# Optimization experiments

Hardware: AMD Instinct MI355X
Metric: run time of the kernel (lower is better)

Reference implementation:

```python
import jax, jax.numpy as jnp
import numpy as np

D_MODEL = 512
NUM_HEADS = 8
DEPTH = D_MODEL // NUM_HEADS


def setup_inputs() -> dict:
    key = jax.random.key(0)
    ks = jax.random.split(key, 11)
    B, S = 2, 4096
    scale = 1.0 / np.sqrt(D_MODEL)
    inp = {
        "q": jax.random.normal(ks[0], (B, S, D_MODEL), jnp.float32),
        "k": jax.random.normal(ks[1], (B, S, D_MODEL), jnp.float32),
        "v": jax.random.normal(ks[2], (B, S, D_MODEL), jnp.float32),
        "wq_w": jax.random.normal(ks[3], (D_MODEL, D_MODEL), jnp.float32) * scale,
        "wq_b": jnp.zeros((D_MODEL,), jnp.float32),
        "wk_w": jax.random.normal(ks[4], (D_MODEL, D_MODEL), jnp.float32) * scale,
        "wk_b": jnp.zeros((D_MODEL,), jnp.float32),
        "wv_w": jax.random.normal(ks[5], (D_MODEL, D_MODEL), jnp.float32) * scale,
        "wv_b": jnp.zeros((D_MODEL,), jnp.float32),
        "wo_w": jax.random.normal(ks[6], (D_MODEL, D_MODEL), jnp.float32) * scale,
        "wo_b": jnp.zeros((D_MODEL,), jnp.float32),
    }
    return inp


def _split_heads(x):
    # [B, S, D] -> [B, H, S, depth]
    B, S, _ = x.shape
    return x.reshape(B, S, NUM_HEADS, DEPTH).transpose(0, 2, 1, 3)


def reference(q, k, v, wq_w, wq_b, wk_w, wk_b, wv_w, wv_b, wo_w, wo_b):
    B, S, _ = q.shape
    qh = _split_heads(q @ wq_w.T + wq_b)  # [B,H,S,d]
    kh = _split_heads(k @ wk_w.T + wk_b)
    vh = _split_heads(v @ wv_w.T + wv_b)
    logits = jnp.einsum('bhqd,bhkd->bhqk', qh, kh) / jnp.sqrt(
        jnp.asarray(DEPTH, jnp.float32))
    attn = jax.nn.softmax(logits, axis=-1)
    out = jnp.einsum('bhqk,bhkd->bhqd', attn, vh)  # [B,H,S,d]
    out = out.transpose(0, 2, 1, 3).reshape(B, S, D_MODEL)
    return out @ wo_w.T + wo_b
```

## Files before the change

### kernel.cpp

```cpp
#include <hip/hip_runtime.h>

typedef __attribute__((ext_vector_type(8))) short short8;
typedef __attribute__((ext_vector_type(4))) float float4v;

#define D_MODEL 512
#define NUM_HEADS 8
#define DEPTH 64
#define SEQ 4096
#define BATCH 2
#define MROWS (BATCH * SEQ)
#define SCALE_Q 0.18033688011112043f

#define SW(r, c) (((r) * 64) + ((((c) ^ ((r) & 7))) * 8))

static __device__ __forceinline__ unsigned short f2bf(float f) {
  unsigned int u = __builtin_bit_cast(unsigned int, f);
  u += 0x7FFFu + ((u >> 16) & 1u);
  return (unsigned short)(u >> 16);
}
static __device__ __forceinline__ unsigned int pk2(float a, float b) {
  return (unsigned int)f2bf(a) | ((unsigned int)f2bf(b) << 16);
}

struct CvtArgs {
  const float4v* src[7];
  uint2* dst[7];
  int n4[7];
};
__global__ __launch_bounds__(256) void cvt_all(CvtArgs a) {
  const int ti = blockIdx.y;
  const float4v* __restrict__ s = a.src[ti];
  uint2* __restrict__ d = a.dst[ti];
  const int n = a.n4[ti];
  for (int i = blockIdx.x * 256 + threadIdx.x; i < n; i += gridDim.x * 256) {
    float4v f = s[i];
    d[i] = make_uint2(pk2(f[0], f[1]), pk2(f[2], f[3]));
  }
}

struct QkvArgs {
  const void* X[3];
  const void* W[3];
  const float* bias[3];
  unsigned short* out[3];
};
template <int XFP32, int WFP32>
__global__ __launch_bounds__(256) void gemm_qkv(QkvArgs a) {
  __shared__ unsigned short As[64 * 72];
  __shared__ unsigned short Bs[64 * 72];
  const int z = blockIdx.z;
  const void* __restrict__ Xv = a.X[z];
  const void* __restrict__ Wv = a.W[z];
  const float* __restrict__ bias = a.bias[z];
  unsigned short* __restrict__ outv = a.out[z];
  const int t = threadIdx.x;
  const int w = t >> 6, l = t & 63, lq = l >> 4, lm = l & 15;
  const int mBase = blockIdx.x * 64;
  const int nBase = blockIdx.y * 64;
  float4v acc[4] = {};
  for (int kc = 0; kc < D_MODEL; kc += 64) {
    __syncthreads();
#pragma unroll
    for (int p = 0; p < 2; ++p) {
      int idx = p * 256 + t;
      int r = idx >> 3, c = (idx & 7) * 8;
      if (XFP32) {
        const float* Xf = (const float*)Xv;
        float4v f0 = *reinterpret_cast<const float4v*>(&Xf[(size_t)(mBase + r) * D_MODEL + kc + c]);
        float4v f1 = *reinterpret_cast<const float4v*>(&Xf[(size_t)(mBase + r) * D_MODEL + kc + c + 4]);
        short8 s;
#pragma unroll
        for (int j = 0; j < 4; ++j) {
          s[j] = (short)f2bf(f0[j]);
          s[4 + j] = (short)f2bf(f1[j]);
        }
        *reinterpret_cast<short8*>(&As[r * 72 + c]) = s;
      } else {
        const unsigned short* Xb = (const unsigned short*)Xv;
        *reinterpret_cast<short8*>(&As[r * 72 + c]) =
            *reinterpret_cast<const short8*>(&Xb[(size_t)(mBase + r) * D_MODEL + kc + c]);
      }
      if (WFP32) {
        const float* Wf = (const float*)Wv;
        float4v f0 = *reinterpret_cast<const float4v*>(&Wf[(size_t)(nBase + r) * D_MODEL + kc + c]);
        float4v f1 = *reinterpret_cast<const float4v*>(&Wf[(size_t)(nBase + r) * D_MODEL + kc + c + 4]);
        short8 s;
#pragma unroll
        for (int j = 0; j < 4; ++j) {
          s[j] = (short)f2bf(f0[j]);
          s[4 + j] = (short)f2bf(f1[j]);
        }
        *reinterpret_cast<short8*>(&Bs[r * 72 + c]) = s;
      } else {
        const unsigned short* Wb = (const unsigned short*)Wv;
        *reinterpret_cast<short8*>(&Bs[r * 72 + c]) =
            *reinterpret_cast<const short8*>(&Wb[(size_t)(nBase + r) * D_MODEL + kc + c]);
      }
    }
    __syncthreads();
#pragma unroll
    for (int kk = 0; kk < 64; kk += 32) {
      short8 av = *reinterpret_cast<const short8*>(&As[(w * 16 + lm) * 72 + kk + lq * 8]);
#pragma unroll
      for (int f = 0; f < 4; ++f) {
        short8 b = *reinterpret_cast<const short8*>(&Bs[(f * 16 + lm) * 72 + kk + lq * 8]);
        acc[f] = __builtin_amdgcn_mfma_f32_16x16x32_bf16(av, b, acc[f], 0, 0, 0);
      }
    }
  }
  if (z == 2) {
    __syncthreads();
    unsigned short* T = As;
#pragma unroll
    for (int f = 0; f < 4; ++f) {
      int dl = f * 16 + lm;
      float bv = bias[nBase + dl];
      uint2 u;
      u.x = pk2(acc[f][0] + bv, acc[f][1] + bv);
      u.y = pk2(acc[f][2] + bv, acc[f][3] + bv);
      int chunk = 2 * w + (lq >> 1);
      *reinterpret_cast<uint2*>(&T[SW(dl, chunk) + (lq & 1) * 4]) = u;
    }
    __syncthreads();
    const int bb = mBase >> 12, s0v = mBase & 4095, h = nBase >> 6;
    const size_t vbase = ((size_t)(bb * NUM_HEADS + h)) * DEPTH * SEQ;
#pragma unroll
    for (int p = 0; p < 2; ++p) {
      int idx = p * 256 + t;
      int d = idx >> 3, c = idx & 7;
      *reinterpret_cast<short8*>(&outv[vbase + (size_t)d * SEQ + s0v + c * 8]) =
          *reinterpret_cast<const short8*>(&T[SW(d, c)]);
    }
  } else {
    const float scale = (z == 0) ? SCALE_Q : 1.0f;
#pragma unroll
    for (int f = 0; f < 4; ++f) {
      int gn = nBase + f * 16 + lm;
      float bv = bias[gn];
#pragma unroll
      for (int r = 0; r < 4; ++r) {
        int gm = mBase + w * 16 + lq * 4 + r;
        float v = (acc[f][r] + bv) * scale;
        int bb = gm >> 12, s = gm & 4095;
        int h = gn >> 6, d = gn & 63;
        outv[(((size_t)(bb * NUM_HEADS + h) * SEQ + s) << 6) + d] = f2bf(v);
      }
    }
  }
}

template <int WFP32>
__global__ __launch_bounds__(256) void gemm_out(
    const unsigned short* __restrict__ Xb,
    const void* __restrict__ Wv,
    const float* __restrict__ bias,
    float* __restrict__ out) {
  __shared__ unsigned short As[64 * 72];
  __shared__ unsigned short Bs[64 * 72];
  const int t = threadIdx.x;
  const int w = t >> 6, l = t & 63, lq = l >> 4, lm = l & 15;
  const int mBase = blockIdx.x * 64;
  const int nBase = blockIdx.y * 64;
  float4v acc[4] = {};
  for (int kc = 0; kc < D_MODEL; kc += 64) {
    __syncthreads();
#pragma unroll
    for (int p = 0; p < 2; ++p) {
      int idx = p * 256 + t;
      int r = idx >> 3, c = (idx & 7) * 8;
      *reinterpret_cast<short8*>(&As[r * 72 + c]) =
          *reinterpret_cast<const short8*>(&Xb[(size_t)(mBase + r) * D_MODEL + kc + c]);
      if (WFP32) {
        const float* Wf = (const float*)Wv;
        float4v f0 = *reinterpret_cast<const float4v*>(&Wf[(size_t)(nBase + r) * D_MODEL + kc + c]);
        float4v f1 = *reinterpret_cast<const float4v*>(&Wf[(size_t)(nBase + r) * D_MODEL + kc + c + 4]);
        short8 s;
#pragma unroll
        for (int j = 0; j < 4; ++j) {
          s[j] = (short)f2bf(f0[j]);
          s[4 + j] = (short)f2bf(f1[j]);
        }
        *reinterpret_cast<short8*>(&Bs[r * 72 + c]) = s;
      } else {
        const unsigned short* Wb = (const unsigned short*)Wv;
        *reinterpret_cast<short8*>(&Bs[r * 72 + c]) =
            *reinterpret_cast<const short8*>(&Wb[(size_t)(nBase + r) * D_MODEL + kc + c]);
      }
    }
    __syncthreads();
#pragma unroll
    for (int kk = 0; kk < 64; kk += 32) {
      short8 av = *reinterpret_cast<const short8*>(&As[(w * 16 + lm) * 72 + kk + lq * 8]);
#pragma unroll
      for (int f = 0; f < 4; ++f) {
        short8 b = *reinterpret_cast<const short8*>(&Bs[(f * 16 + lm) * 72 + kk + lq * 8]);
        acc[f] = __builtin_amdgcn_mfma_f32_16x16x32_bf16(av, b, acc[f], 0, 0, 0);
      }
    }
  }
#pragma unroll
  for (int f = 0; f < 4; ++f) {
    int gn = nBase + f * 16 + lm;
    float bv = bias[gn];
#pragma unroll
    for (int r = 0; r < 4; ++r) {
      int gm = mBase + w * 16 + lq * 4 + r;
      out[(size_t)gm * D_MODEL + gn] = acc[f][r] + bv;
    }
  }
}

__global__ __launch_bounds__(256) void attn(
    const unsigned short* __restrict__ Qh,
    const unsigned short* __restrict__ Kh,
    const unsigned short* __restrict__ Vt,
    unsigned short* __restrict__ AO)
{
  __shared__ unsigned short Ksub[2][64 * 64];
  __shared__ unsigned short Vsub[2][64 * 64];
  __shared__ unsigned short Psub[64 * 64];
  const int t = threadIdx.x;
  const int w = t >> 6;
  const int l = t & 63, lq = l >> 4, lm = l & 15;
  const int bh = blockIdx.y;
  const size_t base = (size_t)bh * SEQ * DEPTH;
  const int qbase = blockIdx.x * 64 + w * 16;
  const unsigned short* __restrict__ Kp = Kh + base;
  const unsigned short* __restrict__ Vp = Vt + base;

  short8 qf[2];
#pragma unroll
  for (int kk = 0; kk < 2; ++kk)
    qf[kk] = *reinterpret_cast<const short8*>(
        &Qh[base + (size_t)(qbase + lm) * DEPTH + kk * 32 + lq * 8]);

  float4v oacc[4] = {};
  float lsum = 0.f;
  short8 kreg[2], vreg[2];

#pragma unroll
  for (int p = 0; p < 2; ++p) {
    int idx = p * 256 + t;
    int r = idx >> 3, c = idx & 7;
    kreg[p] = *reinterpret_cast<const short8*>(&Kp[(size_t)r * DEPTH + c * 8]);
    vreg[p] = *reinterpret_cast<const short8*>(&Vp[(size_t)r * SEQ + c * 8]);
  }
#pragma unroll
  for (int p = 0; p < 2; ++p) {
    int idx = p * 256 + t;
    int r = idx >> 3, c = idx & 7;
    *reinterpret_cast<short8*>(&Ksub[0][SW(r, c)]) = kreg[p];
    *reinterpret_cast<short8*>(&Vsub[0][SW(r, c)]) = vreg[p];
  }
  __syncthreads();

  for (int it = 0; it < 64; ++it) {
    const int cur = it & 1;
    if (it < 63) {
      const int s0n = (it + 1) * 64;
#pragma unroll
      for (int p = 0; p < 2; ++p) {
        int idx = p * 256 + t;
        int r = idx >> 3, c = idx & 7;
        kreg[p] = *reinterpret_cast<const short8*>(&Kp[(size_t)(s0n + r) * DEPTH + c * 8]);
        vreg[p] = *reinterpret_cast<const short8*>(&Vp[(size_t)r * SEQ + s0n + c * 8]);
      }
    }
#pragma unroll
    for (int f = 0; f < 4; ++f) {
      float4v sacc = {};
#pragma unroll
      for (int kk = 0; kk < 2; ++kk) {
        short8 a = *reinterpret_cast<const short8*>(&Ksub[cur][SW(f * 16 + lm, kk * 4 + lq)]);
        sacc = __builtin_amdgcn_mfma_f32_16x16x32_bf16(a, qf[kk], sacc, 0, 0, 0);
      }
      float p0 = exp2f(sacc[0]);
      float p1 = exp2f(sacc[1]);
      float p2 = exp2f(sacc[2]);
      float p3 = exp2f(sacc[3]);
      lsum += (p0 + p1) + (p2 + p3);
      uint2 u;
      u.x = pk2(p0, p1);
      u.y = pk2(p2, p3);
      *reinterpret_cast<uint2*>(&Psub[SW(w * 16 + lm, 2 * f + (lq >> 1)) + (lq & 1) * 4]) = u;
    }
#pragma unroll
    for (int kk = 0; kk < 2; ++kk) {
      short8 a = *reinterpret_cast<const short8*>(&Psub[SW(w * 16 + lm, kk * 4 + lq)]);
#pragma unroll
      for (int df = 0; df < 4; ++df) {
        short8 b = *reinterpret_cast<const short8*>(&Vsub[cur][SW(df * 16 + lm, kk * 4 + lq)]);
        oacc[df] = __builtin_amdgcn_mfma_f32_16x16x32_bf16(a, b, oacc[df], 0, 0, 0);
      }
    }
    if (it < 63) {
#pragma unroll
      for (int p = 0; p < 2; ++p) {
        int idx = p * 256 + t;
        int r = idx >> 3, c = idx & 7;
        *reinterpret_cast<short8*>(&Ksub[cur ^ 1][SW(r, c)]) = kreg[p];
        *reinterpret_cast<short8*>(&Vsub[cur ^ 1][SW(r, c)]) = vreg[p];
      }
    }
    __syncthreads();
  }
  float v = lsum;
  v += __shfl_xor(v, 16);
  v += __shfl_xor(v, 32);
  float rinv = 1.0f / v;
  const int bb = bh >> 3, h = bh & 7;
#pragma unroll
  for (int r = 0; r < 4; ++r) {
    float rq = __shfl(rinv, lq * 4 + r);
    int s = qbase + lq * 4 + r;
#pragma unroll
    for (int df = 0; df < 4; ++df) {
      int d = df * 16 + lm;
      AO[((size_t)(bb * SEQ + s)) * D_MODEL + h * DEPTH + d] = f2bf(oacc[df][r] * rq);
    }
  }
}

extern "C" void kernel_launch(void* const* d_in, const int* in_sizes, int n_in,
                              void* d_out, int out_size, void* d_ws, size_t ws_size,
                              hipStream_t stream) {
  const void* q = d_in[0];
  const void* k = d_in[1];
  const void* v = d_in[2];
  const float* wq = (const float*)d_in[3];
  const float* bq = (const float*)d_in[4];
  const float* wk = (const float*)d_in[5];
  const float* bk = (const float*)d_in[6];
  const float* wv = (const float*)d_in[7];
  const float* bv = (const float*)d_in[8];
  const float* wo = (const float*)d_in[9];
  const float* bo = (const float*)d_in[10];

  const size_t HSD = (size_t)BATCH * NUM_HEADS * SEQ * DEPTH;
  const size_t WSZ = (size_t)D_MODEL * D_MODEL;
  unsigned short* ws = (unsigned short*)d_ws;
  unsigned short* Qh = ws;
  unsigned short* Kh = Qh + HSD;
  unsigned short* Vt = Kh + HSD;
  unsigned short* AO = Vt + HSD;
  unsigned short* Wc[4] = {AO + HSD, AO + HSD + WSZ, AO + HSD + 2 * WSZ, AO + HSD + 3 * WSZ};
  unsigned short* Xc[3] = {Wc[3] + WSZ, Wc[3] + WSZ + HSD, Wc[3] + WSZ + 2 * HSD};
  const int tier = (ws_size >= (7 * HSD + 4 * WSZ) * 2) ? 1
                 : (ws_size >= (4 * HSD + 4 * WSZ) * 2) ? 2 : 3;

  const float* wptr[4] = {wq, wk, wv, wo};
  const void* xin[3] = {q, k, v};

  if (tier < 3) {
    CvtArgs ca = {};
    int ny = 0;
    if (tier == 1) {
      for (int i = 0; i < 3; ++i) {
        ca.src[ny] = (const float4v*)xin[i];
        ca.dst[ny] = (uint2*)Xc[i];
        ca.n4[ny++] = (int)(HSD / 4);
      }
    }
    for (int i = 0; i < 4; ++i) {
      ca.src[ny] = (const float4v*)wptr[i];
      ca.dst[ny] = (uint2*)Wc[i];
      ca.n4[ny++] = (int)(WSZ / 4);
    }
    cvt_all<<<dim3(512, ny), 256, 0, stream>>>(ca);
  }

  QkvArgs qa;
  qa.bias[0] = bq; qa.bias[1] = bk; qa.bias[2] = bv;
  qa.out[0] = Qh; qa.out[1] = Kh; qa.out[2] = Vt;
  dim3 gGrid(MROWS / 64, D_MODEL / 64, 3);
  if (tier == 1) {
    for (int i = 0; i < 3; ++i) { qa.X[i] = Xc[i]; qa.W[i] = Wc[i]; }
    gemm_qkv<0, 0><<<gGrid, 256, 0, stream>>>(qa);
  } else if (tier == 2) {
    for (int i = 0; i < 3; ++i) { qa.X[i] = xin[i]; qa.W[i] = Wc[i]; }
    gemm_qkv<1, 0><<<gGrid, 256, 0, stream>>>(qa);
  } else {
    for (int i = 0; i < 3; ++i) { qa.X[i] = xin[i]; qa.W[i] = wptr[i]; }
    gemm_qkv<1, 1><<<gGrid, 256, 0, stream>>>(qa);
  }

  attn<<<dim3(SEQ / 64, BATCH * NUM_HEADS), 256, 0, stream>>>(Qh, Kh, Vt, AO);

  dim3 oGrid(MROWS / 64, D_MODEL / 64);
  if (tier < 3)
    gemm_out<0><<<oGrid, 256, 0, stream>>>(AO, Wc[3], bo, (float*)d_out);
  else
    gemm_out<1><<<oGrid, 256, 0, stream>>>(AO, wo, bo, (float*)d_out);
}
```

Measured before the change: 287.9 us.

## Use 128x128 GEMM tiles and 128-query attention blocks with MFMA row sums

Adds 128x128-tile bf16 GEMM kernels, each wave computing a 64x64 sub-tile, for the QKV and output projections on the bf16 path. The attention kernel now handles 32 query rows per wave, so each K/V tile loaded into LDS is reused for twice as many queries. Softmax row sums are computed with an MFMA against a vector of ones instead of shuffle reductions, and the exp/pack steps use hardware exp2 and a perm-based bf16 pack. The costs are higher register pressure and LDS use, a grid of half as many attention blocks, and slightly different rounding in the bf16 pack.

```diff
diff --git a/kernel.cpp b/kernel.cpp
--- a/kernel.cpp
+++ b/kernel.cpp
@@ -8,10 +8,11 @@
 #define DEPTH 64
 #define SEQ 4096
 #define BATCH 2
-#define MROWS (BATCH * SEQ)
+#define MROWS 8192
 #define SCALE_Q 0.18033688011112043f
 
 #define SW(r, c) (((r) * 64) + ((((c) ^ ((r) & 7))) * 8))
+#define SW128(n, c) (((n) * 128) + ((((c) ^ ((n) & 15))) * 8))
 
 static __device__ __forceinline__ unsigned short f2bf(float f) {
   unsigned int u = __builtin_bit_cast(unsigned int, f);
@@ -20,6 +21,11 @@
 }
 static __device__ __forceinline__ unsigned int pk2(float a, float b) {
   return (unsigned int)f2bf(a) | ((unsigned int)f2bf(b) << 16);
+}
+static __device__ __forceinline__ unsigned int pk2f(float a, float b) {
+  unsigned int ua = __builtin_bit_cast(unsigned int, a) + 0x8000u;
+  unsigned int ub = __builtin_bit_cast(unsigned int, b) + 0x8000u;
+  return __builtin_amdgcn_perm(ub, ua, 0x07060302u);
 }
 
 struct CvtArgs {
@@ -39,13 +45,153 @@
 }
 
 struct QkvArgs {
+  const unsigned short* X[3];
+  const unsigned short* W[3];
+  const float* bias[3];
+  unsigned short* out[3];
+};
+__global__ __launch_bounds__(256) void gemm128_qkv(QkvArgs a) {
+  __shared__ unsigned short smem[2 * 128 * 64];
+  unsigned short* As = smem;
+  unsigned short* Bs = smem + 128 * 64;
+  const int z = blockIdx.z;
+  const unsigned short* __restrict__ X = a.X[z];
+  const unsigned short* __restrict__ W = a.W[z];
+  const float* __restrict__ bias = a.bias[z];
+  unsigned short* __restrict__ out = a.out[z];
+  const int t = threadIdx.x;
+  const int w = t >> 6, l = t & 63, lq = l >> 4, lm = l & 15;
+  const int mq = (w & 1) * 64, nq = (w >> 1) * 64;
+  const int mBase = blockIdx.x * 128, nBase = blockIdx.y * 128;
+  float4v acc[4][4] = {};
+  for (int kc = 0; kc < D_MODEL; kc += 64) {
+    __syncthreads();
+#pragma unroll
+    for (int p = 0; p < 4; ++p) {
+      int i = p * 256 + t, r = i >> 3, c = i & 7;
+      *(short8*)&As[SW(r, c)] = *(const short8*)&X[(size_t)(mBase + r) * D_MODEL + kc + c * 8];
+      *(short8*)&Bs[SW(r, c)] = *(const short8*)&W[(size_t)(nBase + r) * D_MODEL + kc + c * 8];
+    }
+    __syncthreads();
+#pragma unroll
+    for (int kk = 0; kk < 2; ++kk) {
+      short8 av[4];
+#pragma unroll
+      for (int fm = 0; fm < 4; ++fm)
+        av[fm] = *(const short8*)&As[SW(mq + fm * 16 + lm, kk * 4 + lq)];
+#pragma unroll
+      for (int fn = 0; fn < 4; ++fn) {
+        short8 bv = *(const short8*)&Bs[SW(nq + fn * 16 + lm, kk * 4 + lq)];
+#pragma unroll
+        for (int fm = 0; fm < 4; ++fm)
+          acc[fm][fn] = __builtin_amdgcn_mfma_f32_16x16x32_bf16(av[fm], bv, acc[fm][fn], 0, 0, 0);
+      }
+    }
+  }
+  if (z == 2) {
+    __syncthreads();
+    unsigned short* T = smem;
+#pragma unroll
+    for (int fn = 0; fn < 4; ++fn) {
+      int n = nq + fn * 16 + lm;
+      float bv = bias[nBase + n];
+#pragma unroll
+      for (int fm = 0; fm < 4; ++fm) {
+        int m0 = mq + fm * 16 + lq * 4;
+        uint2 u;
+        u.x = pk2(acc[fm][fn][0] + bv, acc[fm][fn][1] + bv);
+        u.y = pk2(acc[fm][fn][2] + bv, acc[fm][fn][3] + bv);
+        *(uint2*)&T[SW128(n, m0 >> 3) + (lq & 1) * 4] = u;
+      }
+    }
+    __syncthreads();
+    const int bb = mBase >> 12, s0 = mBase & 4095;
+#pragma unroll
+    for (int p = 0; p < 8; ++p) {
+      int i = p * 256 + t, n = i >> 4, cm = i & 15;
+      int gn = nBase + n, h = gn >> 6, d = gn & 63;
+      *(short8*)&out[(((size_t)(bb * NUM_HEADS + h) * DEPTH + d) << 12) + s0 + cm * 8] =
+          *(const short8*)&T[SW128(n, cm)];
+    }
+  } else {
+    const float scale = (z == 0) ? SCALE_Q : 1.0f;
+#pragma unroll
+    for (int fn = 0; fn < 4; ++fn) {
+      int gn = nBase + nq + fn * 16 + lm;
+      float bv = bias[gn];
+      int h = gn >> 6, d = gn & 63;
+#pragma unroll
+      for (int fm = 0; fm < 4; ++fm) {
+#pragma unroll
+        for (int r = 0; r < 4; ++r) {
+          int gm = mBase + mq + fm * 16 + lq * 4 + r;
+          int bb = gm >> 12, s = gm & 4095;
+          out[(((size_t)(bb * NUM_HEADS + h) * SEQ + s) << 6) + d] =
+              f2bf((acc[fm][fn][r] + bv) * scale);
+        }
+      }
+    }
+  }
+}
+
+__global__ __launch_bounds__(256) void gemm128_out(
+    const unsigned short* __restrict__ X, const unsigned short* __restrict__ W,
+    const float* __restrict__ bias, float* __restrict__ out) {
+  __shared__ unsigned short smem[2 * 128 * 64];
+  unsigned short* As = smem;
+  unsigned short* Bs = smem + 128 * 64;
+  const int t = threadIdx.x;
+  const int w = t >> 6, l = t & 63, lq = l >> 4, lm = l & 15;
+  const int mq = (w & 1) * 64, nq = (w >> 1) * 64;
+  const int mBase = blockIdx.x * 128, nBase = blockIdx.y * 128;
+  float4v acc[4][4] = {};
+  for (int kc = 0; kc < D_MODEL; kc += 64) {
+    __syncthreads();
+#pragma unroll
+    for (int p = 0; p < 4; ++p) {
+      int i = p * 256 + t, r = i >> 3, c = i & 7;
+      *(short8*)&As[SW(r, c)] = *(const short8*)&X[(size_t)(mBase + r) * D_MODEL + kc + c * 8];
+      *(short8*)&Bs[SW(r, c)] = *(const short8*)&W[(size_t)(nBase + r) * D_MODEL + kc + c * 8];
+    }
+    __syncthreads();
+#pragma unroll
+    for (int kk = 0; kk < 2; ++kk) {
+      short8 av[4];
+#pragma unroll
+      for (int fm = 0; fm < 4; ++fm)
+        av[fm] = *(const short8*)&As[SW(mq + fm * 16 + lm, kk * 4 + lq)];
+#pragma unroll
+      for (int fn = 0; fn < 4; ++fn) {
+        short8 bv = *(const short8*)&Bs[SW(nq + fn * 16 + lm, kk * 4 + lq)];
+#pragma unroll
+        for (int fm = 0; fm < 4; ++fm)
+          acc[fm][fn] = __builtin_amdgcn_mfma_f32_16x16x32_bf16(av[fm], bv, acc[fm][fn], 0, 0, 0);
+      }
+    }
+  }
+#pragma unroll
+  for (int fn = 0; fn < 4; ++fn) {
+    int gn = nBase + nq + fn * 16 + lm;
+    float bv = bias[gn];
+#pragma unroll
+    for (int fm = 0; fm < 4; ++fm) {
+#pragma unroll
+      for (int r = 0; r < 4; ++r) {
+        int gm = mBase + mq + fm * 16 + lq * 4 + r;
+        out[(size_t)gm * D_MODEL + gn] = acc[fm][fn][r] + bv;
+      }
+    }
+  }
+}
+
+struct QkvArgsF {
   const void* X[3];
   const void* W[3];
   const float* bias[3];
   unsigned short* out[3];
 };
 template <int XFP32, int WFP32>
-__global__ __launch_bounds__(256) void gemm_qkv(QkvArgs a) {
+__global__ __launch_bounds__(256) void gemm_qkv(QkvArgsF a) {
   __shared__ unsigned short As[64 * 72];
   __shared__ unsigned short Bs[64 * 72];
   const int z = blockIdx.z;
@@ -66,44 +212,36 @@
       int r = idx >> 3, c = (idx & 7) * 8;
       if (XFP32) {
         const float* Xf = (const float*)Xv;
-        float4v f0 = *reinterpret_cast<const float4v*>(&Xf[(size_t)(mBase + r) * D_MODEL + kc + c]);
-        float4v f1 = *reinterpret_cast<const float4v*>(&Xf[(size_t)(mBase + r) * D_MODEL + kc + c + 4]);
+        float4v f0 = *(const float4v*)&Xf[(size_t)(mBase + r) * D_MODEL + kc + c];
+        float4v f1 = *(const float4v*)&Xf[(size_t)(mBase + r) * D_MODEL + kc + c + 4];
         short8 s;
 #pragma unroll
-        for (int j = 0; j < 4; ++j) {
-          s[j] = (short)f2bf(f0[j]);
-          s[4 + j] = (short)f2bf(f1[j]);
-        }
-        *reinterpret_cast<short8*>(&As[r * 72 + c]) = s;
+        for (int j = 0; j < 4; ++j) { s[j] = (short)f2bf(f0[j]); s[4 + j] = (short)f2bf(f1[j]); }
+        *(short8*)&As[r * 72 + c] = s;
       } else {
-        const unsigned short* Xb = (const unsigned short*)Xv;
-        *reinterpret_cast<short8*>(&As[r * 72 + c]) =
-            *reinterpret_cast<const short8*>(&Xb[(size_t)(mBase + r) * D_MODEL + kc + c]);
+        *(short8*)&As[r * 72 + c] =
+            *(const short8*)&((const unsigned short*)Xv)[(size_t)(mBase + r) * D_MODEL + kc + c];
       }
       if (WFP32) {
         const float* Wf = (const float*)Wv;
-        float4v f0 = *reinterpret_cast<const float4v*>(&Wf[(size_t)(nBase + r) * D_MODEL + kc + c]);
-        float4v f1 = *reinterpret_cast<const float4v*>(&Wf[(size_t)(nBase + r) * D_MODEL + kc + c + 4]);
+        float4v f0 = *(const float4v*)&Wf[(size_t)(nBase + r) * D_MODEL + kc + c];
+        float4v f1 = *(const float4v*)&Wf[(size_t)(nBase + r) * D_MODEL + kc + c + 4];
         short8 s;
 #pragma unroll
-        for (int j = 0; j < 4; ++j) {
-          s[j] = (short)f2bf(f0[j]);
-          s[4 + j] = (short)f2bf(f1[j]);
-        }
-        *reinterpret_cast<short8*>(&Bs[r * 72 + c]) = s;
+        for (int j = 0; j < 4; ++j) { s[j] = (short)f2bf(f0[j]); s[4 + j] = (short)f2bf(f1[j]); }
+        *(short8*)&Bs[r * 72 + c] = s;
       } else {
-        const unsigned short* Wb = (const unsigned short*)Wv;
-        *reinterpret_cast<short8*>(&Bs[r * 72 + c]) =
-            *reinterpret_cast<const short8*>(&Wb[(size_t)(nBase + r) * D_MODEL + kc + c]);
+        *(short8*)&Bs[r * 72 + c] =
+            *(const short8*)&((const unsigned short*)Wv)[(size_t)(nBase + r) * D_MODEL + kc + c];
       }
     }
     __syncthreads();
 #pragma unroll
     for (int kk = 0; kk < 64; kk += 32) {
-      short8 av = *reinterpret_cast<const short8*>(&As[(w * 16 + lm) * 72 + kk + lq * 8]);
+      short8 av = *(const short8*)&As[(w * 16 + lm) * 72 + kk + lq * 8];
 #pragma unroll
       for (int f = 0; f < 4; ++f) {
-        short8 b = *reinterpret_cast<const short8*>(&Bs[(f * 16 + lm) * 72 + kk + lq * 8]);
+        short8 b = *(const short8*)&Bs[(f * 16 + lm) * 72 + kk + lq * 8];
         acc[f] = __builtin_amdgcn_mfma_f32_16x16x32_bf16(av, b, acc[f], 0, 0, 0);
       }
     }
@@ -119,7 +257,7 @@
       u.x = pk2(acc[f][0] + bv, acc[f][1] + bv);
       u.y = pk2(acc[f][2] + bv, acc[f][3] + bv);
       int chunk = 2 * w + (lq >> 1);
-      *reinterpret_cast<uint2*>(&T[SW(dl, chunk) + (lq & 1) * 4]) = u;
+      *(uint2*)&T[SW(dl, chunk) + (lq & 1) * 4] = u;
     }
     __syncthreads();
     const int bb = mBase >> 12, s0v = mBase & 4095, h = nBase >> 6;
@@ -128,8 +266,7 @@
     for (int p = 0; p < 2; ++p) {
       int idx = p * 256 + t;
       int d = idx >> 3, c = idx & 7;
-      *reinterpret_cast<short8*>(&outv[vbase + (size_t)d * SEQ + s0v + c * 8]) =
-          *reinterpret_cast<const short8*>(&T[SW(d, c)]);
+      *(short8*)&outv[vbase + (size_t)d * SEQ + s0v + c * 8] = *(const short8*)&T[SW(d, c)];
     }
   } else {
     const float scale = (z == 0) ? SCALE_Q : 1.0f;
@@ -149,12 +286,9 @@
   }
 }
 
-template <int WFP32>
-__global__ __launch_bounds__(256) void gemm_out(
-    const unsigned short* __restrict__ Xb,
-    const void* __restrict__ Wv,
-    const float* __restrict__ bias,
-    float* __restrict__ out) {
+__global__ __launch_bounds__(256) void gemm_out_f(
+    const unsigned short* __restrict__ Xb, const float* __restrict__ Wf,
+    const float* __restrict__ bias, float* __restrict__ out) {
   __shared__ unsigned short As[64 * 72];
   __shared__ unsigned short Bs[64 * 72];
   const int t = threadIdx.x;
@@ -168,32 +302,22 @@
     for (int p = 0; p < 2; ++p) {
       int idx = p * 256 + t;
       int r = idx >> 3, c = (idx & 7) * 8;
-      *reinterpret_cast<short8*>(&As[r * 72 + c]) =
-          *reinterpret_cast<const short8*>(&Xb[(size_t)(mBase + r) * D_MODEL + kc + c]);
-      if (WFP32) {
-        const float* Wf = (const float*)Wv;
-        float4v f0 = *reinterpret_cast<const float4v*>(&Wf[(size_t)(nBase + r) * D_MODEL + kc + c]);
-        float4v f1 = *reinterpret_cast<const float4v*>(&Wf[(size_t)(nBase + r) * D_MODEL + kc + c + 4]);
-        short8 s;
-#pragma unroll
-        for (int j = 0; j < 4; ++j) {
-          s[j] = (short)f2bf(f0[j]);
-          s[4 + j] = (short)f2bf(f1[j]);
-        }
-        *reinterpret_cast<short8*>(&Bs[r * 72 + c]) = s;
-      } else {
-        const unsigned short* Wb = (const unsigned short*)Wv;
-        *reinterpret_cast<short8*>(&Bs[r * 72 + c]) =
-            *reinterpret_cast<const short8*>(&Wb[(size_t)(nBase + r) * D_MODEL + kc + c]);
-      }
+      *(short8*)&As[r * 72 + c] =
+          *(const short8*)&Xb[(size_t)(mBase + r) * D_MODEL + kc + c];
+      float4v f0 = *(const float4v*)&Wf[(size_t)(nBase + r) * D_MODEL + kc + c];
+      float4v f1 = *(const float4v*)&Wf[(size_t)(nBase + r) * D_MODEL + kc + c + 4];
+      short8 s;
+#pragma unroll
+      for (int j = 0; j < 4; ++j) { s[j] = (short)f2bf(f0[j]); s[4 + j] = (short)f2bf(f1[j]); }
+      *(short8*)&Bs[r * 72 + c] = s;
     }
     __syncthreads();
 #pragma unroll
     for (int kk = 0; kk < 64; kk += 32) {
-      short8 av = *reinterpret_cast<const short8*>(&As[(w * 16 + lm) * 72 + kk + lq * 8]);
+      short8 av = *(const short8*)&As[(w * 16 + lm) * 72 + kk + lq * 8];
 #pragma unroll
       for (int f = 0; f < 4; ++f) {
-        short8 b = *reinterpret_cast<const short8*>(&Bs[(f * 16 + lm) * 72 + kk + lq * 8]);
+        short8 b = *(const short8*)&Bs[(f * 16 + lm) * 72 + kk + lq * 8];
         acc[f] = __builtin_amdgcn_mfma_f32_16x16x32_bf16(av, b, acc[f], 0, 0, 0);
       }
     }
@@ -218,39 +342,42 @@
 {
   __shared__ unsigned short Ksub[2][64 * 64];
   __shared__ unsigned short Vsub[2][64 * 64];
-  __shared__ unsigned short Psub[64 * 64];
+  __shared__ unsigned short Psub[128 * 64];
   const int t = threadIdx.x;
   const int w = t >> 6;
   const int l = t & 63, lq = l >> 4, lm = l & 15;
   const int bh = blockIdx.y;
   const size_t base = (size_t)bh * SEQ * DEPTH;
-  const int qbase = blockIdx.x * 64 + w * 16;
+  const int qbase = blockIdx.x * 128 + w * 32;
   const unsigned short* __restrict__ Kp = Kh + base;
   const unsigned short* __restrict__ Vp = Vt + base;
 
-  short8 qf[2];
-#pragma unroll
-  for (int kk = 0; kk < 2; ++kk)
-    qf[kk] = *reinterpret_cast<const short8*>(
-        &Qh[base + (size_t)(qbase + lm) * DEPTH + kk * 32 + lq * 8]);
-
-  float4v oacc[4] = {};
-  float lsum = 0.f;
+  short8 qf[2][2];
+#pragma unroll
+  for (int qb = 0; qb < 2; ++qb)
+#pragma unroll
+    for (int kk = 0; kk < 2; ++kk)
+      qf[qb][kk] = *(const short8*)&Qh[base + (size_t)(qbase + qb * 16 + lm) * DEPTH + kk * 32 + lq * 8];
+
+  short8 ones;
+#pragma unroll
+  for (int j = 0; j < 8; ++j) ones[j] = (short)0x3F80;
+
+  float4v oacc[2][4] = {};
+  float4v sumacc[2] = {};
   short8 kreg[2], vreg[2];
 
 #pragma unroll
   for (int p = 0; p < 2; ++p) {
-    int idx = p * 256 + t;
-    int r = idx >> 3, c = idx & 7;
-    kreg[p] = *reinterpret_cast<const short8*>(&Kp[(size_t)r * DEPTH + c * 8]);
-    vreg[p] = *reinterpret_cast<const short8*>(&Vp[(size_t)r * SEQ + c * 8]);
+    int i = p * 256 + t, r = i >> 3, c = i & 7;
+    kreg[p] = *(const short8*)&Kp[(size_t)r * DEPTH + c * 8];
+    vreg[p] = *(const short8*)&Vp[(size_t)r * SEQ + c * 8];
   }
 #pragma unroll
   for (int p = 0; p < 2; ++p) {
-    int idx = p * 256 + t;
-    int r = idx >> 3, c = idx & 7;
-    *reinterpret_cast<short8*>(&Ksub[0][SW(r, c)]) = kreg[p];
-    *reinterpret_cast<short8*>(&Vsub[0][SW(r, c)]) = vreg[p];
+    int i = p * 256 + t, r = i >> 3, c = i & 7;
+    *(short8*)&Ksub[0][SW(r, c)] = kreg[p];
+    *(short8*)&Vsub[0][SW(r, c)] = vreg[p];
   }
   __syncthreads();
 
@@ -260,63 +387,63 @@
       const int s0n = (it + 1) * 64;
 #pragma unroll
       for (int p = 0; p < 2; ++p) {
-        int idx = p * 256 + t;
-        int r = idx >> 3, c = idx & 7;
-        kreg[p] = *reinterpret_cast<const short8*>(&Kp[(size_t)(s0n + r) * DEPTH + c * 8]);
-        vreg[p] = *reinterpret_cast<const short8*>(&Vp[(size_t)r * SEQ + s0n + c * 8]);
+        int i = p * 256 + t, r = i >> 3, c = i & 7;
+        kreg[p] = *(const short8*)&Kp[(size_t)(s0n + r) * DEPTH + c * 8];
+        vreg[p] = *(const short8*)&Vp[(size_t)r * SEQ + s0n + c * 8];
       }
     }
 #pragma unroll
     for (int f = 0; f < 4; ++f) {
-      float4v sacc = {};
+      float4v sacc[2] = {};
 #pragma unroll
       for (int kk = 0; kk < 2; ++kk) {
-        short8 a = *reinterpret_cast<const short8*>(&Ksub[cur][SW(f * 16 + lm, kk * 4 + lq)]);
-        sacc = __builtin_amdgcn_mfma_f32_16x16x32_bf16(a, qf[kk], sacc, 0, 0, 0);
-      }
-      float p0 = exp2f(sacc[0]);
-      float p1 = exp2f(sacc[1]);
-      float p2 = exp2f(sacc[2]);
-      float p3 = exp2f(sacc[3]);
-      lsum += (p0 + p1) + (p2 + p3);
-      uint2 u;
-      u.x = pk2(p0, p1);
-      u.y = pk2(p2, p3);
-      *reinterpret_cast<uint2*>(&Psub[SW(w * 16 + lm, 2 * f + (lq >> 1)) + (lq & 1) * 4]) = u;
+        short8 a = *(const short8*)&Ksub[cur][SW(f * 16 + lm, kk * 4 + lq)];
+        sacc[0] = __builtin_amdgcn_mfma_f32_16x16x32_bf16(a, qf[0][kk], sacc[0], 0, 0, 0);
+        sacc[1] = __builtin_amdgcn_mfma_f32_16x16x32_bf16(a, qf[1][kk], sacc[1], 0, 0, 0);
+      }
+#pragma unroll
+      for (int qb = 0; qb < 2; ++qb) {
+        uint2 u;
+        u.x = pk2f(__builtin_amdgcn_exp2f(sacc[qb][0]), __builtin_amdgcn_exp2f(sacc[qb][1]));
+        u.y = pk2f(__builtin_amdgcn_exp2f(sacc[qb][2]), __builtin_amdgcn_exp2f(sacc[qb][3]));
+        *(uint2*)&Psub[SW(w * 32 + qb * 16 + lm, 2 * f + (lq >> 1)) + (lq & 1) * 4] = u;
+      }
     }
 #pragma unroll
     for (int kk = 0; kk < 2; ++kk) {
-      short8 a = *reinterpret_cast<const short8*>(&Psub[SW(w * 16 + lm, kk * 4 + lq)]);
+      short8 a0 = *(const short8*)&Psub[SW(w * 32 + lm, kk * 4 + lq)];
+      short8 a1 = *(const short8*)&Psub[SW(w * 32 + 16 + lm, kk * 4 + lq)];
+      sumacc[0] = __builtin_amdgcn_mfma_f32_16x16x32_bf16(a0, ones, sumacc[0], 0, 0, 0);
+      sumacc[1] = __builtin_amdgcn_mfma_f32_16x16x32_bf16(a1, ones, sumacc[1], 0, 0, 0);
 #pragma unroll
       for (int df = 0; df < 4; ++df) {
-        short8 b = *reinterpret_cast<const short8*>(&Vsub[cur][SW(df * 16 + lm, kk * 4 + lq)]);
-        oacc[df] = __builtin_amdgcn_mfma_f32_16x16x32_bf16(a, b, oacc[df], 0, 0, 0);
+        short8 b = *(const short8*)&Vsub[cur][SW(df * 16 + lm, kk * 4 + lq)];
+        oacc[0][df] = __builtin_amdgcn_mfma_f32_16x16x32_bf16(a0, b, oacc[0][df], 0, 0, 0);
+        oacc[1][df] = __builtin_amdgcn_mfma_f32_16x16x32_bf16(a1, b, oacc[1][df], 0, 0, 0);
       }
     }
     if (it < 63) {
 #pragma unroll
       for (int p = 0; p < 2; ++p) {
-        int idx = p * 256 + t;
-        int r = idx >> 3, c = idx & 7;
-        *reinterpret_cast<short8*>(&Ksub[cur ^ 1][SW(r, c)]) = kreg[p];
-        *reinterpret_cast<short8*>(&Vsub[cur ^ 1][SW(r, c)]) = vreg[p];
-      }
-    }
-    __syncthreads();
-  }
-  float v = lsum;
-  v += __shfl_xor(v, 16);
-  v += __shfl_xor(v, 32);
-  float rinv = 1.0f / v;
+        int i = p * 256 + t, r = i >> 3, c = i & 7;
+        *(short8*)&Ksub[cur ^ 1][SW(r, c)] = kreg[p];
+        *(short8*)&Vsub[cur ^ 1][SW(r, c)] = vreg[p];
+      }
+    }
+    __syncthreads();
+  }
   const int bb = bh >> 3, h = bh & 7;
 #pragma unroll
-  for (int r = 0; r < 4; ++r) {
-    float rq = __shfl(rinv, lq * 4 + r);
-    int s = qbase + lq * 4 + r;
-#pragma unroll
-    for (int df = 0; df < 4; ++df) {
-      int d = df * 16 + lm;
-      AO[((size_t)(bb * SEQ + s)) * D_MODEL + h * DEPTH + d] = f2bf(oacc[df][r] * rq);
+  for (int qb = 0; qb < 2; ++qb) {
+#pragma unroll
+    for (int r = 0; r < 4; ++r) {
+      float rinv = 1.0f / sumacc[qb][r];
+      int s = qbase + qb * 16 + lq * 4 + r;
+#pragma unroll
+      for (int df = 0; df < 4; ++df) {
+        int d = df * 16 + lm;
+        AO[((size_t)(bb * SEQ + s)) * D_MODEL + h * DEPTH + d] = f2bf(oacc[qb][df][r] * rinv);
+      }
     }
   }
 }
@@ -369,26 +496,31 @@
     cvt_all<<<dim3(512, ny), 256, 0, stream>>>(ca);
   }
 
-  QkvArgs qa;
-  qa.bias[0] = bq; qa.bias[1] = bk; qa.bias[2] = bv;
-  qa.out[0] = Qh; qa.out[1] = Kh; qa.out[2] = Vt;
-  dim3 gGrid(MROWS / 64, D_MODEL / 64, 3);
   if (tier == 1) {
+    QkvArgs qa;
     for (int i = 0; i < 3; ++i) { qa.X[i] = Xc[i]; qa.W[i] = Wc[i]; }
-    gemm_qkv<0, 0><<<gGrid, 256, 0, stream>>>(qa);
-  } else if (tier == 2) {
-    for (int i = 0; i < 3; ++i) { qa.X[i] = xin[i]; qa.W[i] = Wc[i]; }
-    gemm_qkv<1, 0><<<gGrid, 256, 0, stream>>>(qa);
+    qa.bias[0] = bq; qa.bias[1] = bk; qa.bias[2] = bv;
+    qa.out[0] = Qh; qa.out[1] = Kh; qa.out[2] = Vt;
+    gemm128_qkv<<<dim3(MROWS / 128, D_MODEL / 128, 3), 256, 0, stream>>>(qa);
   } else {
-    for (int i = 0; i < 3; ++i) { qa.X[i] = xin[i]; qa.W[i] = wptr[i]; }
-    gemm_qkv<1, 1><<<gGrid, 256, 0, stream>>>(qa);
-  }
-
-  attn<<<dim3(SEQ / 64, BATCH * NUM_HEADS), 256, 0, stream>>>(Qh, Kh, Vt, AO);
-
-  dim3 oGrid(MROWS / 64, D_MODEL / 64);
+    QkvArgsF qa;
+    for (int i = 0; i < 3; ++i) qa.X[i] = xin[i];
+    qa.bias[0] = bq; qa.bias[1] = bk; qa.bias[2] = bv;
+    qa.out[0] = Qh; qa.out[1] = Kh; qa.out[2] = Vt;
+    dim3 g(MROWS / 64, D_MODEL / 64, 3);
+    if (tier == 2) {
+      for (int i = 0; i < 3; ++i) qa.W[i] = Wc[i];
+      gemm_qkv<1, 0><<<g, 256, 0, stream>>>(qa);
+    } else {
+      for (int i = 0; i < 3; ++i) qa.W[i] = wptr[i];
+      gemm_qkv<1, 1><<<g, 256, 0, stream>>>(qa);
+    }
+  }
+
+  attn<<<dim3(SEQ / 128, BATCH * NUM_HEADS), 256, 0, stream>>>(Qh, Kh, Vt, AO);
+
   if (tier < 3)
-    gemm_out<0><<<oGrid, 256, 0, stream>>>(AO, Wc[3], bo, (float*)d_out);
+    gemm128_out<<<dim3(MROWS / 128, D_MODEL / 128), 256, 0, stream>>>(AO, Wc[3], bo, (float*)d_out);
   else
-    gemm_out<1><<<oGrid, 256, 0, stream>>>(AO, wo, bo, (float*)d_out);
-}
+    gemm_out_f<<<dim3(MROWS / 64, D_MODEL / 64), 256, 0, stream>>>(AO, wo, bo, (float*)d_out);
+}
```

Result: faster. 243.8 us (-15.3%).
